# Kernel tuning notes

Hardware: AMD Instinct MI355X
Metric: run time of the kernel (lower is better)

The kernel has to match this reference:

```python
import jax, jax.numpy as jnp
import numpy as np

# dims (see shape_source)
N = 20000      # spots / graph nodes
G = 3000       # genes
NF = 256       # NFeature = CrossAttention dim
D_IN = 256     # dims_spot[0]
HID = 64       # dims_spot[1]
OUT = 16       # dims_spot[2]
H = 3          # GATv2 heads
E1 = 640000
E2 = 320000
SLOPE = 0.2    # leaky relu negative slope (GATv2 + CrossAttention alpha)


def _gat_params(key, din, hid, heads):
    k = jax.random.split(key, 3)
    s = 1.0 / np.sqrt(din)
    Wl = jax.random.normal(k[0], (din, heads * hid), jnp.float32) * s
    Wr = jax.random.normal(k[1], (din, heads * hid), jnp.float32) * s
    att = jax.random.normal(k[2], (heads, hid), jnp.float32) * s
    bl = jnp.zeros((heads * hid,), jnp.float32)
    br = jnp.zeros((heads * hid,), jnp.float32)
    b = jnp.zeros((hid,), jnp.float32)
    return Wl, bl, Wr, br, att, b


def setup_inputs() -> dict:
    key = jax.random.key(0)
    ks = jax.random.split(key, 16)
    inp = {
        "gene_freq_mtx": jax.random.normal(ks[0], (NF, G), jnp.float32),
        "gene_eigvecs_T": jax.random.normal(ks[1], (G, N), jnp.float32) / np.sqrt(G),
        "spot_freq_mtx": jax.random.normal(ks[2], (N, D_IN), jnp.float32),
        "spot_eigvecs_T": jax.random.normal(ks[3], (D_IN, NF), jnp.float32) / np.sqrt(D_IN),
        "spotnet": jax.random.randint(ks[4], (2, E1), 0, N, jnp.int32),
        "spotnet_cluster": jax.random.randint(ks[5], (2, E2), 0, N, jnp.int32),
    }
    for name, din, kk in [("c1", D_IN, ks[6]), ("c1p", D_IN, ks[7]), ("c3", OUT, ks[8]), ("c3p", OUT, ks[9])]:
        Wl, bl, Wr, br, att, b = _gat_params(kk, din, HID, H)
        inp[name + "_Wl"] = Wl; inp[name + "_bl"] = bl
        inp[name + "_Wr"] = Wr; inp[name + "_br"] = br
        inp[name + "_att"] = att; inp[name + "_b"] = b
    inp["W2"] = jax.random.normal(ks[10], (2 * HID, OUT), jnp.float32) / np.sqrt(2 * HID)
    inp["b2"] = jnp.zeros((OUT,), jnp.float32)
    inp["W4"] = jax.random.normal(ks[11], (2 * HID, D_IN), jnp.float32) / np.sqrt(2 * HID)
    inp["b4"] = jnp.zeros((D_IN,), jnp.float32)
    inp["a1"] = jax.random.normal(ks[12], (2 * NF, 1), jnp.float32) * 0.05
    inp["a2"] = jax.random.normal(ks[13], (2 * NF, 1), jnp.float32) * 0.05
    return inp


def gatv2(x, edge_index, Wl, bl, Wr, br, att, b, n):
    """PyG GATv2Conv, concat=False (head mean), add_self_loops=False, eval mode."""
    heads, c = att.shape
    src, dst = edge_index[0], edge_index[1]
    xl = (x @ Wl + bl).reshape(-1, heads, c)   # source transform [N,H,C]
    xr = (x @ Wr + br).reshape(-1, heads, c)   # target transform [N,H,C]
    m = jax.nn.leaky_relu(xl[src] + xr[dst], SLOPE)          # [E,H,C]
    e = jnp.einsum('ehc,hc->eh', m, att)                      # [E,H]
    emax = jax.ops.segment_max(e, dst, num_segments=n)        # [N,H]
    emax = jnp.where(jnp.isfinite(emax), emax, 0.0)           # empty segments
    p = jnp.exp(e - emax[dst])
    denom = jax.ops.segment_sum(p, dst, num_segments=n)       # [N,H]
    alpha = p / jnp.maximum(denom, 1e-16)[dst]                # segment softmax
    out = jax.ops.segment_sum(alpha[:, :, None] * xl[src], dst, num_segments=n)
    return out.mean(axis=1) + b                                # [N,C]


def reference(gene_freq_mtx, gene_eigvecs_T, spot_freq_mtx, spot_eigvecs_T,
              c1_Wl, c1_bl, c1_Wr, c1_br, c1_att, c1_b,
              c1p_Wl, c1p_bl, c1p_Wr, c1p_br, c1p_att, c1p_b,
              W2, b2,
              c3_Wl, c3_bl, c3_Wr, c3_br, c3_att, c3_b,
              c3p_Wl, c3p_bl, c3p_Wr, c3p_br, c3p_att, c3p_b,
              W4, b4, a1, a2, spotnet, spotnet_cluster):
    n = spot_freq_mtx.shape[0]
    # GAT (cluster=True)
    h1n = gatv2(spot_freq_mtx, spotnet, c1_Wl, c1_bl, c1_Wr, c1_br, c1_att, c1_b, n)
    h1p = gatv2(spot_freq_mtx, spotnet_cluster, c1p_Wl, c1p_bl, c1p_Wr, c1p_br, c1p_att, c1p_b, n)
    h1 = jax.nn.elu(jnp.concatenate([h1n, h1p], axis=1))
    h2 = h1 @ W2 + b2                                          # emb_spot [N,OUT]
    h3n = gatv2(h2, spotnet, c3_Wl, c3_bl, c3_Wr, c3_br, c3_att, c3_b, n)
    h3p = gatv2(h2, spotnet_cluster, c3p_Wl, c3p_bl, c3p_Wr, c3p_br, c3p_att, c3p_b, n)
    h3 = jax.nn.elu(jnp.concatenate([h3n, h3p], axis=1))
    h4 = h3 @ W4 + b4                                          # mtx_res_spot [N,D_IN]
    # iGFT + clip-at-zero (== relu)
    Xg = jax.nn.relu(gene_eigvecs_T.T @ gene_freq_mtx.T)       # [N,NF]
    Xs = jax.nn.relu(h4 @ spot_eigvecs_T)                      # [N,NF]
    # CrossAttention (dropout=0.0)
    cat = jnp.concatenate([Xg, Xs], axis=1)                    # [N,2NF]
    e = jax.nn.leaky_relu(jnp.concatenate([cat @ a1, cat @ a2], axis=1), SLOPE)
    lam = jax.nn.softmax(e, axis=1)                            # [N,2]
    res = lam[:, :1] * Xg + lam[:, 1:] * Xs
    return (res, lam, h2, h4)
```

## Files before the change

### kernel.cpp

```cpp
#include <hip/hip_runtime.h>

typedef unsigned short u16;
typedef __attribute__((ext_vector_type(8))) short bf16x8;
typedef __attribute__((ext_vector_type(4))) float floatx4;

#define NSPOT 20000
#define NGENE 3000
#define E1N   640000
#define E2N   320000

#define OFF_RES 0
#define OFF_LAM 5120000
#define OFF_H2  5160000
#define OFF_H4  5480000

__device__ __forceinline__ float b2f(u16 u){
  union { unsigned int i; float f; } v; v.i = ((unsigned int)u) << 16; return v.f;
}
__device__ __forceinline__ u16 f2b(float f){
  union { float f; unsigned int i; } v; v.f = f;
  unsigned int i = v.i;
  return (u16)((i + 0x7FFFu + ((i >> 16) & 1u)) >> 16);
}
__device__ __forceinline__ void stout(void* O, size_t i, float v, int isbf){
  if (isbf) ((u16*)O)[i] = f2b(v); else ((float*)O)[i] = v;
}
__device__ __forceinline__ u16 ldu(const void* p, size_t i, int isbf){
  return isbf ? ((const u16*)p)[i] : f2b(((const float*)p)[i]);
}

__global__ void sniff_kernel(const u16* __restrict__ x, int* __restrict__ flag){
  int lane = threadIdx.x;
  u16 u = x[lane * 2];
  int e = (u >> 7) & 0xFF;
  int sane = (u == 0) || (e >= 0x60 && e <= 0xA0);
  unsigned long long b = __ballot(sane);
  if (lane == 0) flag[0] = (__popcll(b) >= 48) ? 1 : 0;
}

struct ConvSeg { const void* src; u16* dst; int n; };
struct ConvBatch { ConvSeg s[14]; };
__global__ void convbatch_kernel(ConvBatch cb, const int* __restrict__ dflag){
  ConvSeg S = cb.s[blockIdx.y];
  int i = blockIdx.x * 256 + threadIdx.x;
  if (i < S.n) S.dst[i] = ldu(S.src, i, dflag[0]);
}

__global__ void conv3_kernel(const void* __restrict__ s0, u16* __restrict__ d0, int n0,
                             const void* __restrict__ s1, u16* __restrict__ d1, int n1,
                             const void* __restrict__ s2, u16* __restrict__ d2, int n2,
                             const int* __restrict__ dflag){
  int i = blockIdx.x * 256 + threadIdx.x;
  const void* src; u16* dst; int local;
  if (i < n0){ src = s0; dst = d0; local = i; }
  else if (i < n0 + n1){ src = s1; dst = d1; local = i - n0; }
  else if (i < n0 + n1 + n2){ src = s2; dst = d2; local = i - n0 - n1; }
  else return;
  size_t b = (size_t)local * 4;
  u16 o[4];
  if (dflag[0]){
    *(uint2*)o = *(const uint2*)((const u16*)src + b);
  } else {
    float4 f = *(const float4*)((const float*)src + b);
    o[0]=f2b(f.x); o[1]=f2b(f.y); o[2]=f2b(f.z); o[3]=f2b(f.w);
  }
  *(uint2*)(dst + b) = *(uint2*)o;
}

__global__ __launch_bounds__(256) void transpose_kernel(
    const void* __restrict__ GE, u16* __restrict__ AT,
    const int* __restrict__ dflag, int K, int M){
  __shared__ float tile[64 * 65];
  int isbf = dflag[0];
  int m0 = blockIdx.x * 64, k0 = blockIdx.y * 64;
#pragma unroll
  for (int i = 0; i < 4; i++){
    int idx = threadIdx.x + i * 256;
    int kr = idx >> 4, mc = (idx & 15) * 4;
    int gk = k0 + kr, gm = m0 + mc;
    if (gk < K){
      float v0 = 0.f, v1 = 0.f, v2 = 0.f, v3 = 0.f;
      if (gm + 4 <= M){
        if (isbf){
          const u16* pp = (const u16*)GE + (size_t)gk * M + gm;
          v0 = b2f(pp[0]); v1 = b2f(pp[1]); v2 = b2f(pp[2]); v3 = b2f(pp[3]);
        } else {
          float4 f = *(const float4*)((const float*)GE + (size_t)gk * M + gm);
          v0 = f.x; v1 = f.y; v2 = f.z; v3 = f.w;
        }
      } else {
        for (int e = 0; e < 4; e++){
          if (gm + e < M){
            float t = isbf ? b2f(((const u16*)GE)[(size_t)gk * M + gm + e])
                           : ((const float*)GE)[(size_t)gk * M + gm + e];
            if (e == 0) v0 = t; else if (e == 1) v1 = t; else if (e == 2) v2 = t; else v3 = t;
          }
        }
      }
      tile[(mc + 0) * 65 + kr] = v0;
      tile[(mc + 1) * 65 + kr] = v1;
      tile[(mc + 2) * 65 + kr] = v2;
      tile[(mc + 3) * 65 + kr] = v3;
    }
  }
  __syncthreads();
#pragma unroll
  for (int i = 0; i < 2; i++){
    int idx = threadIdx.x + i * 256;
    int mr = idx >> 3, kc = (idx & 7) * 8;
    int gm = m0 + mr, gk = k0 + kc;
    if (gm < M && gk < K){
      if (gk + 8 <= K){
        u16 o[8];
#pragma unroll
        for (int e = 0; e < 8; e++) o[e] = f2b(tile[mr * 65 + kc + e]);
        *(uint4*)&AT[(size_t)gm * K + gk] = *(uint4*)o;
      } else {
        for (int e = 0; e < 8 && gk + e < K; e++)
          AT[(size_t)gm * K + gk + e] = f2b(tile[mr * 65 + kc + e]);
      }
    }
  }
}

__global__ void hist2_kernel(const int* __restrict__ dst0, int E0, int* __restrict__ cnt0,
                             const int* __restrict__ dst1, int E1, int* __restrict__ cnt1){
  const int* dst = blockIdx.y ? dst1 : dst0;
  int* cnt = blockIdx.y ? cnt1 : cnt0;
  int E = blockIdx.y ? E1 : E0;
  int e = blockIdx.x * 256 + threadIdx.x;
  if (e < E){ int d = dst[e]; if ((unsigned)d < (unsigned)NSPOT) atomicAdd(&cnt[d], 1); }
}

__global__ void scan2_kernel(const int* __restrict__ c0, int* __restrict__ o0, int* __restrict__ u0,
                             const int* __restrict__ c1, int* __restrict__ o1, int* __restrict__ u1,
                             int n){
  const int* cnt = blockIdx.x ? c1 : c0;
  int* off = blockIdx.x ? o1 : o0;
  int* cur = blockIdx.x ? u1 : u0;
  __shared__ int part[256];
  int tid = threadIdx.x;
  int chunk = (n + 255) / 256;
  int lo = tid * chunk; if (lo > n) lo = n;
  int hi = lo + chunk; if (hi > n) hi = n;
  int s = 0;
  for (int i = lo; i < hi; i++) s += cnt[i];
  part[tid] = s;
  __syncthreads();
  if (tid == 0){
    int run = 0;
    for (int i = 0; i < 256; i++){ int t = part[i]; part[i] = run; run += t; }
  }
  __syncthreads();
  int run = part[tid];
  for (int i = lo; i < hi; i++){ off[i] = run; cur[i] = run; run += cnt[i]; }
  if (hi == n) off[n] = run;
}

__global__ void scatter2_kernel(const int* __restrict__ src0, const int* __restrict__ dst0,
                                int* __restrict__ cur0, int* __restrict__ out0, int E0,
                                const int* __restrict__ src1, const int* __restrict__ dst1,
                                int* __restrict__ cur1, int* __restrict__ out1, int E1){
  const int* src = blockIdx.y ? src1 : src0;
  const int* dst = blockIdx.y ? dst1 : dst0;
  int* cur = blockIdx.y ? cur1 : cur0;
  int* out = blockIdx.y ? out1 : out0;
  int E = blockIdx.y ? E1 : E0;
  int e = blockIdx.x * 256 + threadIdx.x;
  if (e < E){
    int d = dst[e];
    if ((unsigned)d < (unsigned)NSPOT){
      int p = atomicAdd(&cur[d], 1);
      if ((unsigned)p < (unsigned)E) out[p] = src[e];
    }
  }
}

struct AsmSet {
  const void *Wl, *bl, *Wr, *br, *Wlp, *blp, *Wrp, *brp;
  u16* Wcat; u16* bcat; int Kdim;
};
__global__ void assemble2_kernel(AsmSet s0, AsmSet s1, const int* __restrict__ dflag){
  AsmSet S = blockIdx.y ? s1 : s0;
  int isbf = dflag[0];
  int idx = blockIdx.x * 256 + threadIdx.x;
  int total = S.Kdim * 768;
  if (idx < total){
    int k = idx / 768, j = idx % 768;
    int seg = j / 192, jj = j % 192;
    const void* W = (seg == 0) ? S.Wl : (seg == 1) ? S.Wr : (seg == 2) ? S.Wlp : S.Wrp;
    S.Wcat[idx] = ldu(W, (size_t)k * 192 + jj, isbf);
  }
  if (idx < 768){
    int seg = idx / 192, jj = idx % 192;
    const void* b = (seg == 0) ? S.bl : (seg == 1) ? S.br : (seg == 2) ? S.blp : S.brp;
    S.bcat[idx] = ldu(b, jj, isbf);
  }
}

template<int BMI, bool A_KM, bool B_NK, bool A_EXT, bool B_EXT, bool RELU, bool HAS_BIAS, bool C_OUT, bool C2>
__global__ __launch_bounds__(256) void gemm_mfma(
    const void* __restrict__ A, const void* __restrict__ B,
    const u16* __restrict__ bias, void* __restrict__ Cp, u16* __restrict__ Cp2,
    const int* __restrict__ dflag, size_t aoff, size_t coff,
    int M, int N, int K, int lda, int ldb, int ldc, int ldc2)
{
  const int isbf = dflag[0];
  constexpr int BM = 64 * BMI, BK = 32, LDA = BK + 8, LDB = BK + 8;
  __shared__ __align__(16) u16 As[BM * LDA];
  __shared__ __align__(16) u16 Bs[64 * LDB];
  const u16*   A16 = (const u16*)A + aoff;
  const float* A32 = (const float*)A + aoff;
  const u16*   B16 = (const u16*)B;
  const float* B32 = (const float*)B;
  auto ldA = [&](size_t i) -> u16 { return (!A_EXT || isbf) ? A16[i] : f2b(A32[i]); };
  auto ldB = [&](size_t i) -> u16 { return (!B_EXT || isbf) ? B16[i] : f2b(B32[i]); };

  int tid = threadIdx.x;
  int lane = tid & 63, w = tid >> 6;
  int m0 = blockIdx.y * BM, n0 = blockIdx.x * 64;
  floatx4 acc[BMI][4] = {};
  int quad = lane >> 4;
  int nk = (K + BK - 1) / BK;
  for (int kt = 0; kt < nk; kt++){
    int k0 = kt * BK;
    if (!A_KM){
#pragma unroll
      for (int i = 0; i < BMI; i++){
        int id = tid + i * 256;
        int r = id >> 2, c = (id & 3) * 8;
        int gm = m0 + r, gk = k0 + c;
        if (gm < M && gk + 8 <= K){
          if (!A_EXT || isbf){
            *(uint4*)&As[r * LDA + c] = *(const uint4*)(A16 + (size_t)gm * lda + gk);
          } else {
            const float* p = A32 + (size_t)gm * lda + gk;
            float4 f0 = *(const float4*)p, f1 = *(const float4*)(p + 4);
            u16* d = &As[r * LDA + c];
            d[0]=f2b(f0.x); d[1]=f2b(f0.y); d[2]=f2b(f0.z); d[3]=f2b(f0.w);
            d[4]=f2b(f1.x); d[5]=f2b(f1.y); d[6]=f2b(f1.z); d[7]=f2b(f1.w);
          }
        } else {
          for (int e = 0; e < 8; e++)
            As[r * LDA + c + e] = (gm < M && gk + e < K) ? ldA((size_t)gm * lda + gk + e) : (u16)0;
        }
      }
    } else {
#pragma unroll
      for (int i = 0; i < BMI; i++){
        int id = tid + i * 256;
        int kk, rr;
        if (BMI == 2){ kk = id >> 4; rr = (id & 15) * 8; }
        else         { kk = id >> 3; rr = (id & 7) * 8; }
        int gk = k0 + kk, gm = m0 + rr;
        if (gk < K && gm + 8 <= M){
          if (!A_EXT || isbf){
            uint4 v = *(const uint4*)(A16 + (size_t)gk * lda + gm);
            const u16* pv = (const u16*)&v;
#pragma unroll
            for (int e = 0; e < 8; e++) As[(rr + e) * LDA + kk] = pv[e];
          } else {
            const float* p = A32 + (size_t)gk * lda + gm;
            float4 f0 = *(const float4*)p, f1 = *(const float4*)(p + 4);
            As[(rr+0)*LDA+kk]=f2b(f0.x); As[(rr+1)*LDA+kk]=f2b(f0.y);
            As[(rr+2)*LDA+kk]=f2b(f0.z); As[(rr+3)*LDA+kk]=f2b(f0.w);
            As[(rr+4)*LDA+kk]=f2b(f1.x); As[(rr+5)*LDA+kk]=f2b(f1.y);
            As[(rr+6)*LDA+kk]=f2b(f1.z); As[(rr+7)*LDA+kk]=f2b(f1.w);
          }
        } else {
          for (int e = 0; e < 8; e++)
            As[(rr + e) * LDA + kk] = (gk < K && gm + e < M) ? ldA((size_t)gk * lda + gm + e) : (u16)0;
        }
      }
    }
    if (B_NK){
      int r = tid >> 2, c = (tid & 3) * 8;
      int gn = n0 + r, gk = k0 + c;
      if (gn < N && gk + 8 <= K){
        if (!B_EXT || isbf){
          *(uint4*)&Bs[r * LDB + c] = *(const uint4*)(B16 + (size_t)gn * ldb + gk);
        } else {
          const float* p = B32 + (size_t)gn * ldb + gk;
          float4 f0 = *(const float4*)p, f1 = *(const float4*)(p + 4);
          u16* d = &Bs[r * LDB + c];
          d[0]=f2b(f0.x); d[1]=f2b(f0.y); d[2]=f2b(f0.z); d[3]=f2b(f0.w);
          d[4]=f2b(f1.x); d[5]=f2b(f1.y); d[6]=f2b(f1.z); d[7]=f2b(f1.w);
        }
      } else {
        for (int e = 0; e < 8; e++)
          Bs[r * LDB + c + e] = (gn < N && gk + e < K) ? ldB((size_t)gn * ldb + gk + e) : (u16)0;
      }
    } else {
      int kk = tid >> 3, nn = (tid & 7) * 8;
      int gk = k0 + kk, gn = n0 + nn;
      if (gk < K && gn + 8 <= N){
        if (!B_EXT || isbf){
          uint4 v = *(const uint4*)(B16 + (size_t)gk * ldb + gn);
          const u16* pv = (const u16*)&v;
#pragma unroll
          for (int e = 0; e < 8; e++) Bs[(nn + e) * LDB + kk] = pv[e];
        } else {
          const float* p = B32 + (size_t)gk * ldb + gn;
          float4 f0 = *(const float4*)p, f1 = *(const float4*)(p + 4);
          Bs[(nn+0)*LDB+kk]=f2b(f0.x); Bs[(nn+1)*LDB+kk]=f2b(f0.y);
          Bs[(nn+2)*LDB+kk]=f2b(f0.z); Bs[(nn+3)*LDB+kk]=f2b(f0.w);
          Bs[(nn+4)*LDB+kk]=f2b(f1.x); Bs[(nn+5)*LDB+kk]=f2b(f1.y);
          Bs[(nn+6)*LDB+kk]=f2b(f1.z); Bs[(nn+7)*LDB+kk]=f2b(f1.w);
        }
      } else {
        for (int e = 0; e < 8; e++)
          Bs[(nn + e) * LDB + kk] = (gk < K && gn + e < N) ? ldB((size_t)gk * ldb + gn + e) : (u16)0;
      }
    }
    __syncthreads();
    bf16x8 af[BMI];
#pragma unroll
    for (int mi = 0; mi < BMI; mi++)
      af[mi] = *(const bf16x8*)&As[(w * (16 * BMI) + mi * 16 + (lane & 15)) * LDA + quad * 8];
#pragma unroll
    for (int ni = 0; ni < 4; ni++){
      bf16x8 bfr = *(const bf16x8*)&Bs[(ni * 16 + (lane & 15)) * LDB + quad * 8];
#pragma unroll
      for (int mi = 0; mi < BMI; mi++)
        acc[mi][ni] = __builtin_amdgcn_mfma_f32_16x16x32_bf16(af[mi], bfr, acc[mi][ni], 0, 0, 0);
    }
    __syncthreads();
  }
#pragma unroll
  for (int mi = 0; mi < BMI; mi++)
#pragma unroll
    for (int ni = 0; ni < 4; ni++)
#pragma unroll
      for (int r = 0; r < 4; r++){
        int row = m0 + w * (16 * BMI) + mi * 16 + quad * 4 + r;
        int col = n0 + ni * 16 + (lane & 15);
        if (row < M && col < N){
          float v = acc[mi][ni][r];
          if (HAS_BIAS) v += b2f(bias[col]);
          if (RELU) v = fmaxf(v, 0.f);
          size_t ci = coff + (size_t)row * ldc + col;
          if (!C_OUT) ((u16*)Cp)[ci] = f2b(v);
          else stout(Cp, ci, v, isbf);
          if (C2) Cp2[(size_t)row * ldc2 + col] = f2b(v);
        }
      }
}

struct GatSet {
  const int* off; const int* srcs; const u16* att; const u16* bias;
  int xl_off, xr_off, out_off, E;
};
__global__ __launch_bounds__(256) void gat2_kernel(
    const u16* __restrict__ Y, GatSet SA, GatSet SB,
    u16* __restrict__ aggout, int n)
{
  int half = gridDim.x >> 1;
  int selB = (int)blockIdx.x >= half;
  GatSet S = selB ? SB : SA;
  int bx = blockIdx.x - (selB ? half : 0);
  int wid = (bx * 256 + threadIdx.x) >> 6;
  int lane = threadIdx.x & 63;
  if (wid >= n) return;
  int sub = lane >> 4;
  int cbase = (lane & 15) * 4;
  const int ldY = 768;
  size_t drow = (size_t)wid * ldY;

  float xr[3][4], at[3][4];
#pragma unroll
  for (int h = 0; h < 3; h++){
    uint2 vx = *(const uint2*)(Y + drow + S.xr_off + h * 64 + cbase);
    uint2 va = *(const uint2*)(S.att + h * 64 + cbase);
    const u16* px = (const u16*)&vx;
    const u16* pa = (const u16*)&va;
#pragma unroll
    for (int j = 0; j < 4; j++){ xr[h][j] = b2f(px[j]); at[h][j] = b2f(pa[j]); }
  }

  int beg = S.off[wid], end = S.off[wid + 1];
  beg = max(0, min(beg, S.E));
  end = max(beg, min(end, S.E));

  float mh[3] = {-INFINITY, -INFINITY, -INFINITY};
  float lh[3] = {0.f, 0.f, 0.f};
  float ac[3][4] = {};

  uint2 xa[3] = {};
  int s_b = 0;
  if (beg < end){
    int e0 = beg + sub;
    int s = (e0 < end) ? S.srcs[e0] : 0;
    if ((unsigned)s >= (unsigned)NSPOT) s = 0;
    const u16* p = Y + (size_t)s * ldY + S.xl_off + cbase;
#pragma unroll
    for (int h = 0; h < 3; h++) xa[h] = *(const uint2*)(p + h * 64);
    if (beg + 4 < end){
      int e1 = beg + 4 + sub;
      int s1 = (e1 < end) ? S.srcs[e1] : 0;
      if ((unsigned)s1 >= (unsigned)NSPOT) s1 = 0;
      s_b = s1;
    }
  }

  for (int b = beg; b < end; b += 4){
    uint2 xc[3];
#pragma unroll
    for (int h = 0; h < 3; h++) xc[h] = xa[h];
    bool act = (b + sub) < end;

    if (b + 4 < end){
      const u16* p = Y + (size_t)s_b * ldY + S.xl_off + cbase;
#pragma unroll
      for (int h = 0; h < 3; h++) xa[h] = *(const uint2*)(p + h * 64);
      if (b + 8 < end){
        int e2 = b + 8 + sub;
        int s2 = (e2 < end) ? S.srcs[e2] : 0;
        if ((unsigned)s2 >= (unsigned)NSPOT) s2 = 0;
        s_b = s2;
      }
    }

    float xl[3][4];
    float t0, t1, t2;
    {
      float a0 = 0.f, a1 = 0.f, a2 = 0.f;
      const u16* p0 = (const u16*)&xc[0];
      const u16* p1 = (const u16*)&xc[1];
      const u16* p2 = (const u16*)&xc[2];
#pragma unroll
      for (int j = 0; j < 4; j++){
        float x0 = b2f(p0[j]); xl[0][j] = x0;
        float u0 = x0 + xr[0][j]; u0 = fmaxf(u0, 0.2f * u0);
        a0 = __builtin_fmaf(at[0][j], u0, a0);
        float x1 = b2f(p1[j]); xl[1][j] = x1;
        float u1 = x1 + xr[1][j]; u1 = fmaxf(u1, 0.2f * u1);
        a1 = __builtin_fmaf(at[1][j], u1, a1);
        float x2 = b2f(p2[j]); xl[2][j] = x2;
        float u2 = x2 + xr[2][j]; u2 = fmaxf(u2, 0.2f * u2);
        a2 = __builtin_fmaf(at[2][j], u2, a2);
      }
      t0 = a0; t1 = a1; t2 = a2;
    }
#pragma unroll
    for (int d = 1; d < 16; d <<= 1){
      t0 += __shfl_xor(t0, d, 64);
      t1 += __shfl_xor(t1, d, 64);
      t2 += __shfl_xor(t2, d, 64);
    }
    if (act){
      float tt[3] = {t0, t1, t2};
#pragma unroll
      for (int h = 0; h < 3; h++){
        float nm = fmaxf(mh[h], tt[h]);
        if (nm > mh[h]){
          float sc = __expf(mh[h] - nm);
          lh[h] *= sc;
#pragma unroll
          for (int j = 0; j < 4; j++) ac[h][j] *= sc;
          mh[h] = nm;
        }
        float w = __expf(tt[h] - mh[h]);
        lh[h] += w;
#pragma unroll
        for (int j = 0; j < 4; j++) ac[h][j] = __builtin_fmaf(w, xl[h][j], ac[h][j]);
      }
    }
  }

  float o[4] = {0.f, 0.f, 0.f, 0.f};
#pragma unroll
  for (int h = 0; h < 3; h++){
    float gm = fmaxf(mh[h], __shfl_xor(mh[h], 16, 64));
    gm = fmaxf(gm, __shfl_xor(gm, 32, 64));
    float sc = (mh[h] == -INFINITY) ? 0.f : __expf(mh[h] - gm);
    float L = lh[h] * sc;
    L += __shfl_xor(L, 16, 64);
    L += __shfl_xor(L, 32, 64);
    float inv = 1.f / fmaxf(L, 1e-16f);
#pragma unroll
    for (int j = 0; j < 4; j++){
      float a = ac[h][j] * sc;
      a += __shfl_xor(a, 16, 64);
      a += __shfl_xor(a, 32, 64);
      o[j] += a * inv;
    }
  }
  if (sub == 0){
    u16 ov[4];
#pragma unroll
    for (int j = 0; j < 4; j++){
      float v = o[j] * (1.f / 3.f) + b2f(S.bias[cbase + j]);
      v = (v > 0.f) ? v : expm1f(v);
      if (!(fabsf(v) < 1e30f)) v = 0.f;
      ov[j] = f2b(v);
    }
    *(uint2*)&aggout[(size_t)wid * 128 + S.out_off + cbase] = *(uint2*)ov;
  }
}

__global__ __launch_bounds__(256) void h2y2_kernel(
    const u16* __restrict__ AGG, const u16* __restrict__ W2, const u16* __restrict__ b2,
    const u16* __restrict__ Wcat2, const u16* __restrict__ bcat2,
    void* __restrict__ OUT, u16* __restrict__ Y2,
    const int* __restrict__ dflag, int n){
  __shared__ float w2s[128 * 16];
  __shared__ float as_[16][128];
  __shared__ float h[16][16];
  __shared__ __align__(16) u16 ws_[16 * 768];
  int isbf = dflag[0];
  int tid = threadIdx.x;
  for (int i = tid; i < 128 * 16; i += 256) w2s[i] = b2f(W2[i]);
  for (int i = tid; i < 1536; i += 256) ((uint4*)ws_)[i] = ((const uint4*)Wcat2)[i];
  int m0 = blockIdx.x * 16;
  for (int i = tid; i < 16 * 128; i += 256){
    int r = i >> 7, c = i & 127; int m = m0 + r;
    as_[r][c] = (m < n) ? b2f(AGG[(size_t)m * 128 + c]) : 0.f;
  }
  __syncthreads();
  {
    int r = tid >> 4, j = tid & 15;
    int m = m0 + r;
    float acc = b2f(b2[j]);
    for (int k = 0; k < 128; k++) acc += as_[r][k] * w2s[k * 16 + j];
    h[r][j] = acc;
    if (m < n) stout(OUT, (size_t)OFF_H2 + (size_t)m * 16 + j, acc, isbf);
  }
  __syncthreads();
  int j = tid;
  float acc[16][3];
  float bj0 = b2f(bcat2[j]), bj1 = b2f(bcat2[j + 256]), bj2 = b2f(bcat2[j + 512]);
#pragma unroll
  for (int r = 0; r < 16; r++){ acc[r][0] = bj0; acc[r][1] = bj1; acc[r][2] = bj2; }
  for (int k = 0; k < 16; k++){
    float w0 = b2f(ws_[k * 768 + j]);
    float w1 = b2f(ws_[k * 768 + j + 256]);
    float w2 = b2f(ws_[k * 768 + j + 512]);
#pragma unroll
    for (int r = 0; r < 16; r++){
      float hv = h[r][k];
      acc[r][0] += hv * w0; acc[r][1] += hv * w1; acc[r][2] += hv * w2;
    }
  }
#pragma unroll
  for (int r = 0; r < 16; r++){
    int m = m0 + r;
    if (m < n){
      size_t base = (size_t)m * 768;
      Y2[base + j] = f2b(acc[r][0]);
      Y2[base + j + 256] = f2b(acc[r][1]);
      Y2[base + j + 512] = f2b(acc[r][2]);
    }
  }
}

__global__ __launch_bounds__(256) void cross_attn_kernel(
    const u16* __restrict__ XG, const u16* __restrict__ XS,
    const u16* __restrict__ a1, const u16* __restrict__ a2,
    void* __restrict__ OUT, const int* __restrict__ dflag, int n){
  int wid = (blockIdx.x * 256 + threadIdx.x) >> 6;
  int lane = threadIdx.x & 63;
  if (wid >= n) return;
  int isbf = dflag[0];
  int c0 = lane * 4;
  size_t base = (size_t)wid * 256 + c0;
  float g[4], s[4];
#pragma unroll
  for (int e = 0; e < 4; e++){ g[e] = b2f(XG[base + e]); s[e] = b2f(XS[base + e]); }
  float p1 = 0.f, p2 = 0.f;
#pragma unroll
  for (int e = 0; e < 4; e++){
    p1 += g[e] * b2f(a1[c0 + e]) + s[e] * b2f(a1[256 + c0 + e]);
    p2 += g[e] * b2f(a2[c0 + e]) + s[e] * b2f(a2[256 + c0 + e]);
  }
#pragma unroll
  for (int d = 32; d > 0; d >>= 1){
    p1 += __shfl_xor(p1, d, 64);
    p2 += __shfl_xor(p2, d, 64);
  }
  float e1 = (p1 > 0.f) ? p1 : 0.2f * p1;
  float e2 = (p2 > 0.f) ? p2 : 0.2f * p2;
  float mx = fmaxf(e1, e2);
  float w1 = __expf(e1 - mx), w2 = __expf(e2 - mx);
  float inv = 1.f / (w1 + w2);
  float l0 = w1 * inv, l1 = w2 * inv;
#pragma unroll
  for (int e = 0; e < 4; e++)
    stout(OUT, (size_t)OFF_RES + base + e, l0 * g[e] + l1 * s[e], isbf);
  if (lane == 0){
    stout(OUT, (size_t)OFF_LAM + (size_t)wid * 2,     l0, isbf);
    stout(OUT, (size_t)OFF_LAM + (size_t)wid * 2 + 1, l1, isbf);
  }
}

extern "C" void kernel_launch(void* const* d_in, const int* in_sizes, int n_in,
                              void* d_out, int out_size, void* d_ws, size_t ws_size,
                              hipStream_t stream) {
  const void* gene_freq = d_in[0];
  const void* gene_eig  = d_in[1];
  const void* spot_freq = d_in[2];
  const void* spot_eig  = d_in[3];
  const int* net1 = (const int*)d_in[4];
  const int* net2 = (const int*)d_in[5];
  const void *c1_Wl=d_in[6],  *c1_bl=d_in[7],  *c1_Wr=d_in[8],  *c1_br=d_in[9],  *c1_att=d_in[10], *c1_b=d_in[11];
  const void *c1p_Wl=d_in[12],*c1p_bl=d_in[13],*c1p_Wr=d_in[14],*c1p_br=d_in[15],*c1p_att=d_in[16],*c1p_b=d_in[17];
  const void *c3_Wl=d_in[18], *c3_bl=d_in[19], *c3_Wr=d_in[20], *c3_br=d_in[21], *c3_att=d_in[22], *c3_b=d_in[23];
  const void *c3p_Wl=d_in[24],*c3p_bl=d_in[25],*c3p_Wr=d_in[26],*c3p_br=d_in[27],*c3p_att=d_in[28],*c3p_b=d_in[29];
  const void *W2=d_in[30], *b2=d_in[31], *W4=d_in[32], *b4=d_in[33], *a1=d_in[34], *a2=d_in[35];

  char* p0 = (char*)d_ws;
  char* p = p0;
  auto carve = [&](size_t bytes) -> char* {
    char* r = p; p += (bytes + 255) & ~(size_t)255; return r;
  };
  int*   flag  = (int*) carve(256);
  int*   cnt1  = (int*) carve((NSPOT + 2) * 4);
  int*   off1  = (int*) carve((NSPOT + 2) * 4);
  int*   cur1  = (int*) carve((NSPOT + 2) * 4);
  int*   srcs1 = (int*) carve((size_t)E1N * 4);
  int*   cnt2  = (int*) carve((NSPOT + 2) * 4);
  int*   off2  = (int*) carve((NSPOT + 2) * 4);
  int*   cur2  = (int*) carve((NSPOT + 2) * 4);
  int*   srcs2 = (int*) carve((size_t)E2N * 4);
  u16*   Wcat1 = (u16*) carve(256 * 768 * 2);
  u16*   bcat1 = (u16*) carve(2048);
  u16*   Wcat2 = (u16*) carve(16 * 768 * 2);
  u16*   bcat2 = (u16*) carve(2048);
  u16*   attc1  = (u16*)carve(192 * 2);
  u16*   attc1p = (u16*)carve(192 * 2);
  u16*   attc3  = (u16*)carve(192 * 2);
  u16*   attc3p = (u16*)carve(192 * 2);
  u16*   bc1  = (u16*)carve(64 * 2);
  u16*   bc1p = (u16*)carve(64 * 2);
  u16*   bc3  = (u16*)carve(64 * 2);
  u16*   bc3p = (u16*)carve(64 * 2);
  u16*   W2c  = (u16*)carve(2048 * 2);
  u16*   b2c  = (u16*)carve(16 * 2);
  u16*   W4c  = (u16*)carve(32768 * 2);
  u16*   b4c  = (u16*)carve(256 * 2);
  u16*   a1c  = (u16*)carve(512 * 2);
  u16*   a2c  = (u16*)carve(512 * 2);
  u16*   GF16 = (u16*) carve((size_t)256 * 3000 * 2);
  u16*   SE16 = (u16*) carve((size_t)256 * 256 * 2);
  u16*   SF16 = (u16*) carve((size_t)NSPOT * 256 * 2);
  u16*   H4B  = (u16*) carve((size_t)NSPOT * 256 * 2);
  u16*   AGG  = (u16*) carve((size_t)NSPOT * 128 * 2);
  u16*   XGp  = (u16*) carve((size_t)NSPOT * 256 * 2);
  char*  R    = carve(0);
  size_t used_common = (size_t)(R - p0);
  size_t needA = used_common + (size_t)NSPOT * NGENE * 2
               + (size_t)NSPOT * 768 * 2
               + (size_t)NSPOT * 256 * 2
               + 4096;
  bool planA = (ws_size >= needA);

  sniff_kernel<<<1, 64, 0, stream>>>((const u16*)spot_freq, flag);
  hipMemsetAsync(cnt1, 0, NSPOT * 4, stream);
  hipMemsetAsync(cnt2, 0, NSPOT * 4, stream);
  hist2_kernel<<<dim3((E1N + 255) / 256, 2), 256, 0, stream>>>(
      net1 + E1N, E1N, cnt1, net2 + E2N, E2N, cnt2);
  scan2_kernel<<<2, 256, 0, stream>>>(cnt1, off1, cur1, cnt2, off2, cur2, NSPOT);
  scatter2_kernel<<<dim3((E1N + 255) / 256, 2), 256, 0, stream>>>(
      net1, net1 + E1N, cur1, srcs1, E1N, net2, net2 + E2N, cur2, srcs2, E2N);

  ConvBatch cb;
  cb.s[0]  = {c1_att,  attc1,  192}; cb.s[1]  = {c1p_att, attc1p, 192};
  cb.s[2]  = {c3_att,  attc3,  192}; cb.s[3]  = {c3p_att, attc3p, 192};
  cb.s[4]  = {c1_b, bc1, 64}; cb.s[5]  = {c1p_b, bc1p, 64};
  cb.s[6]  = {c3_b, bc3, 64}; cb.s[7]  = {c3p_b, bc3p, 64};
  cb.s[8]  = {W2, W2c, 2048}; cb.s[9]  = {b2, b2c, 16};
  cb.s[10] = {W4, W4c, 32768}; cb.s[11] = {b4, b4c, 256};
  cb.s[12] = {a1, a1c, 512}; cb.s[13] = {a2, a2c, 512};
  convbatch_kernel<<<dim3(128, 14), 256, 0, stream>>>(cb, flag);

  {
    int n0 = 256 * 3000 / 4, n1 = 256 * 256 / 4, n2 = NSPOT * 256 / 4;
    int tot = n0 + n1 + n2;
    conv3_kernel<<<(tot + 255) / 256, 256, 0, stream>>>(
        gene_freq, GF16, n0, spot_eig, SE16, n1, spot_freq, SF16, n2, flag);
  }

  AsmSet as0 = {c1_Wl, c1_bl, c1_Wr, c1_br, c1p_Wl, c1p_bl, c1p_Wr, c1p_br, Wcat1, bcat1, 256};
  AsmSet as1 = {c3_Wl, c3_bl, c3_Wr, c3_br, c3p_Wl, c3p_bl, c3p_Wr, c3p_br, Wcat2, bcat2, 16};
  assemble2_kernel<<<dim3((256 * 768 + 255) / 256, 2), 256, 0, stream>>>(as0, as1, flag);

  GatSet g1a = {off1, srcs1, attc1,  bc1,  0,   192, 0,  E1N};
  GatSet g1b = {off2, srcs2, attc1p, bc1p, 384, 576, 64, E2N};
  GatSet g3a = {off1, srcs1, attc3,  bc3,  0,   192, 0,  E1N};
  GatSet g3b = {off2, srcs2, attc3p, bc3p, 384, 576, 64, E2N};

  u16* Y;
  u16* XS;
  u16* XG = XGp;
  if (planA){
    u16* AT = (u16*)R;
    Y  = (u16*)(R + (size_t)NSPOT * NGENE * 2);
    XS = Y + (size_t)NSPOT * 768;

    transpose_kernel<<<dim3(313, 47), 256, 0, stream>>>(gene_eig, AT, flag, NGENE, NSPOT);
    gemm_mfma<2, false, true, false, false, true, false, false, false><<<dim3(4, 157), 256, 0, stream>>>(
        AT, GF16, nullptr, XG, nullptr, flag, 0, 0, NSPOT, 256, NGENE, NGENE, NGENE, 256, 0);
  } else {
    Y  = (u16*)R;
    XS = Y + (size_t)NSPOT * 768;
    gemm_mfma<2, true, true, true, true, true, false, false, false><<<dim3(4, 157), 256, 0, stream>>>(
        gene_eig, gene_freq, nullptr, XG, nullptr, flag, 0, 0, NSPOT, 256, NGENE, NSPOT, NGENE, 256, 0);
  }

  gemm_mfma<2, false, false, false, false, false, true, false, false><<<dim3(12, 157), 256, 0, stream>>>(
      SF16, Wcat1, bcat1, Y, nullptr, flag, 0, 0, NSPOT, 768, 256, 256, 768, 768, 0);
  gat2_kernel<<<10000, 256, 0, stream>>>(Y, g1a, g1b, AGG, NSPOT);
  h2y2_kernel<<<1250, 256, 0, stream>>>(AGG, W2c, b2c, Wcat2, bcat2, d_out, Y, flag, NSPOT);
  gat2_kernel<<<10000, 256, 0, stream>>>(Y, g3a, g3b, AGG, NSPOT);
  gemm_mfma<2, false, false, false, false, false, true, true, true><<<dim3(4, 157), 256, 0, stream>>>(
      AGG, W4c, b4c, d_out, H4B, flag, 0, OFF_H4, NSPOT, 256, 128, 128, 256, 256, 256);
  gemm_mfma<2, false, false, false, false, true, false, false, false><<<dim3(4, 157), 256, 0, stream>>>(
      H4B, SE16, nullptr, XS, nullptr, flag, 0, 0, NSPOT, 256, 256, 256, 256, 256, 0);
  cross_attn_kernel<<<5000, 256, 0, stream>>>(XG, XS, a1c, a2c, d_out, flag, NSPOT);

  (void)in_sizes; (void)n_in; (void)out_size; (void)ws_size;
}
```

Before: 1.091 ms.

## Compute gene iGFT transposed with split-K, drop explicit transpose, widen GAT lanes

```diff
diff --git a/kernel.cpp b/kernel.cpp
--- a/kernel.cpp
+++ b/kernel.cpp
@@ -65,62 +65,6 @@
     o[0]=f2b(f.x); o[1]=f2b(f.y); o[2]=f2b(f.z); o[3]=f2b(f.w);
   }
   *(uint2*)(dst + b) = *(uint2*)o;
-}
-
-__global__ __launch_bounds__(256) void transpose_kernel(
-    const void* __restrict__ GE, u16* __restrict__ AT,
-    const int* __restrict__ dflag, int K, int M){
-  __shared__ float tile[64 * 65];
-  int isbf = dflag[0];
-  int m0 = blockIdx.x * 64, k0 = blockIdx.y * 64;
-#pragma unroll
-  for (int i = 0; i < 4; i++){
-    int idx = threadIdx.x + i * 256;
-    int kr = idx >> 4, mc = (idx & 15) * 4;
-    int gk = k0 + kr, gm = m0 + mc;
-    if (gk < K){
-      float v0 = 0.f, v1 = 0.f, v2 = 0.f, v3 = 0.f;
-      if (gm + 4 <= M){
-        if (isbf){
-          const u16* pp = (const u16*)GE + (size_t)gk * M + gm;
-          v0 = b2f(pp[0]); v1 = b2f(pp[1]); v2 = b2f(pp[2]); v3 = b2f(pp[3]);
-        } else {
-          float4 f = *(const float4*)((const float*)GE + (size_t)gk * M + gm);
-          v0 = f.x; v1 = f.y; v2 = f.z; v3 = f.w;
-        }
-      } else {
-        for (int e = 0; e < 4; e++){
-          if (gm + e < M){
-            float t = isbf ? b2f(((const u16*)GE)[(size_t)gk * M + gm + e])
-                           : ((const float*)GE)[(size_t)gk * M + gm + e];
-            if (e == 0) v0 = t; else if (e == 1) v1 = t; else if (e == 2) v2 = t; else v3 = t;
-          }
-        }
-      }
-      tile[(mc + 0) * 65 + kr] = v0;
-      tile[(mc + 1) * 65 + kr] = v1;
-      tile[(mc + 2) * 65 + kr] = v2;
-      tile[(mc + 3) * 65 + kr] = v3;
-    }
-  }
-  __syncthreads();
-#pragma unroll
-  for (int i = 0; i < 2; i++){
-    int idx = threadIdx.x + i * 256;
-    int mr = idx >> 3, kc = (idx & 7) * 8;
-    int gm = m0 + mr, gk = k0 + kc;
-    if (gm < M && gk < K){
-      if (gk + 8 <= K){
-        u16 o[8];
-#pragma unroll
-        for (int e = 0; e < 8; e++) o[e] = f2b(tile[mr * 65 + kc + e]);
-        *(uint4*)&AT[(size_t)gm * K + gk] = *(uint4*)o;
-      } else {
-        for (int e = 0; e < 8 && gk + e < K; e++)
-          AT[(size_t)gm * K + gk + e] = f2b(tile[mr * 65 + kc + e]);
-      }
-    }
-  }
 }
 
 __global__ void hist2_kernel(const int* __restrict__ dst0, int E0, int* __restrict__ cnt0,
@@ -198,12 +142,13 @@
   }
 }
 
-template<int BMI, bool A_KM, bool B_NK, bool A_EXT, bool B_EXT, bool RELU, bool HAS_BIAS, bool C_OUT, bool C2>
+template<int BMI, bool A_KM, bool B_NK, bool A_EXT, bool B_EXT, bool RELU, bool HAS_BIAS, bool C_OUT, bool C2, bool C_F32>
 __global__ __launch_bounds__(256) void gemm_mfma(
     const void* __restrict__ A, const void* __restrict__ B,
     const u16* __restrict__ bias, void* __restrict__ Cp, u16* __restrict__ Cp2,
     const int* __restrict__ dflag, size_t aoff, size_t coff,
-    int M, int N, int K, int lda, int ldb, int ldc, int ldc2)
+    int M, int N, int K, int kchunk, size_t cstride,
+    int lda, int ldb, int ldc, int ldc2)
 {
   const int isbf = dflag[0];
   constexpr int BM = 64 * BMI, BK = 32, LDA = BK + 8, LDB = BK + 8;
@@ -219,11 +164,13 @@
   int tid = threadIdx.x;
   int lane = tid & 63, w = tid >> 6;
   int m0 = blockIdx.y * BM, n0 = blockIdx.x * 64;
+  int kbeg = (int)blockIdx.z * kchunk;
+  int kend = (K < kbeg + kchunk) ? K : (kbeg + kchunk);
   floatx4 acc[BMI][4] = {};
   int quad = lane >> 4;
-  int nk = (K + BK - 1) / BK;
+  int nk = (kend - kbeg + BK - 1) / BK;
   for (int kt = 0; kt < nk; kt++){
-    int k0 = kt * BK;
+    int k0 = kbeg + kt * BK;
     if (!A_KM){
 #pragma unroll
       for (int i = 0; i < BMI; i++){
@@ -338,12 +285,58 @@
           float v = acc[mi][ni][r];
           if (HAS_BIAS) v += b2f(bias[col]);
           if (RELU) v = fmaxf(v, 0.f);
-          size_t ci = coff + (size_t)row * ldc + col;
-          if (!C_OUT) ((u16*)Cp)[ci] = f2b(v);
+          size_t ci = coff + (size_t)blockIdx.z * cstride + (size_t)row * ldc + col;
+          if (C_F32) ((float*)Cp)[ci] = v;
+          else if (!C_OUT) ((u16*)Cp)[ci] = f2b(v);
           else stout(Cp, ci, v, isbf);
           if (C2) Cp2[(size_t)row * ldc2 + col] = f2b(v);
         }
       }
+}
+
+__global__ __launch_bounds__(256) void redtr_kernel(const float* __restrict__ P,
+                                                    u16* __restrict__ XG){
+  __shared__ float tile[64 * 65];
+  int s0 = blockIdx.x * 64;
+  int c0 = blockIdx.y * 64;
+  int t = threadIdx.x;
+#pragma unroll
+  for (int i = 0; i < 4; i++){
+    int c = i * 16 + (t >> 4);
+    int sp = (t & 15) * 4;
+    int gs = s0 + sp;
+    size_t base = (size_t)(c0 + c) * NSPOT + gs;
+    float v0 = 0.f, v1 = 0.f, v2 = 0.f, v3 = 0.f;
+    if (gs + 4 <= NSPOT){
+      float4 a = *(const float4*)(P + base);
+      float4 b = *(const float4*)(P + (size_t)256 * NSPOT + base);
+      v0 = a.x + b.x; v1 = a.y + b.y; v2 = a.z + b.z; v3 = a.w + b.w;
+    } else {
+      for (int e = 0; e < 4; e++){
+        if (gs + e < NSPOT){
+          float x = P[base + e] + P[(size_t)256 * NSPOT + base + e];
+          if (e == 0) v0 = x; else if (e == 1) v1 = x; else if (e == 2) v2 = x; else v3 = x;
+        }
+      }
+    }
+    tile[c * 65 + sp + 0] = fmaxf(v0, 0.f);
+    tile[c * 65 + sp + 1] = fmaxf(v1, 0.f);
+    tile[c * 65 + sp + 2] = fmaxf(v2, 0.f);
+    tile[c * 65 + sp + 3] = fmaxf(v3, 0.f);
+  }
+  __syncthreads();
+#pragma unroll
+  for (int i = 0; i < 2; i++){
+    int sp = i * 32 + (t >> 3);
+    int cc = (t & 7) * 8;
+    int gs = s0 + sp;
+    if (gs < NSPOT){
+      u16 o[8];
+#pragma unroll
+      for (int e = 0; e < 8; e++) o[e] = f2b(tile[(cc + e) * 65 + sp]);
+      *(uint4*)&XG[(size_t)gs * 256 + c0 + cc] = *(uint4*)o;
+    }
+  }
 }
 
 struct GatSet {
@@ -361,20 +354,20 @@
   int wid = (bx * 256 + threadIdx.x) >> 6;
   int lane = threadIdx.x & 63;
   if (wid >= n) return;
-  int sub = lane >> 4;
-  int cbase = (lane & 15) * 4;
+  int sub = lane >> 3;
+  int cbase = (lane & 7) * 8;
   const int ldY = 768;
   size_t drow = (size_t)wid * ldY;
 
-  float xr[3][4], at[3][4];
+  float xr[3][8], at[3][8];
 #pragma unroll
   for (int h = 0; h < 3; h++){
-    uint2 vx = *(const uint2*)(Y + drow + S.xr_off + h * 64 + cbase);
-    uint2 va = *(const uint2*)(S.att + h * 64 + cbase);
+    uint4 vx = *(const uint4*)(Y + drow + S.xr_off + h * 64 + cbase);
+    uint4 va = *(const uint4*)(S.att + h * 64 + cbase);
     const u16* px = (const u16*)&vx;
     const u16* pa = (const u16*)&va;
 #pragma unroll
-    for (int j = 0; j < 4; j++){ xr[h][j] = b2f(px[j]); at[h][j] = b2f(pa[j]); }
+    for (int j = 0; j < 8; j++){ xr[h][j] = b2f(px[j]); at[h][j] = b2f(pa[j]); }
   }
 
   int beg = S.off[wid], end = S.off[wid + 1];
@@ -383,9 +376,9 @@
 
   float mh[3] = {-INFINITY, -INFINITY, -INFINITY};
   float lh[3] = {0.f, 0.f, 0.f};
-  float ac[3][4] = {};
-
-  uint2 xa[3] = {};
+  float ac[3][8] = {};
+
+  uint4 xa[3] = {};
   int s_b = 0;
   if (beg < end){
     int e0 = beg + sub;
@@ -393,56 +386,54 @@
     if ((unsigned)s >= (unsigned)NSPOT) s = 0;
     const u16* p = Y + (size_t)s * ldY + S.xl_off + cbase;
 #pragma unroll
-    for (int h = 0; h < 3; h++) xa[h] = *(const uint2*)(p + h * 64);
-    if (beg + 4 < end){
-      int e1 = beg + 4 + sub;
+    for (int h = 0; h < 3; h++) xa[h] = *(const uint4*)(p + h * 64);
+    if (beg + 8 < end){
+      int e1 = beg + 8 + sub;
       int s1 = (e1 < end) ? S.srcs[e1] : 0;
       if ((unsigned)s1 >= (unsigned)NSPOT) s1 = 0;
       s_b = s1;
     }
   }
 
-  for (int b = beg; b < end; b += 4){
-    uint2 xc[3];
+  for (int b = beg; b < end; b += 8){
+    uint4 xc[3];
 #pragma unroll
     for (int h = 0; h < 3; h++) xc[h] = xa[h];
     bool act = (b + sub) < end;
 
-    if (b + 4 < end){
+    if (b + 8 < end){
       const u16* p = Y + (size_t)s_b * ldY + S.xl_off + cbase;
 #pragma unroll
-      for (int h = 0; h < 3; h++) xa[h] = *(const uint2*)(p + h * 64);
-      if (b + 8 < end){
-        int e2 = b + 8 + sub;
+      for (int h = 0; h < 3; h++) xa[h] = *(const uint4*)(p + h * 64);
+      if (b + 16 < end){
+        int e2 = b + 16 + sub;
         int s2 = (e2 < end) ? S.srcs[e2] : 0;
         if ((unsigned)s2 >= (unsigned)NSPOT) s2 = 0;
         s_b = s2;
       }
     }
 
-    float xl[3][4];
-    float t0, t1, t2;
+    float xl[3][8];
+    float t0 = 0.f, t1 = 0.f, t2 = 0.f;
     {
-      float a0 = 0.f, a1 = 0.f, a2 = 0.f;
       const u16* p0 = (const u16*)&xc[0];
       const u16* p1 = (const u16*)&xc[1];
       const u16* p2 = (const u16*)&xc[2];
 #pragma unroll
-      for (int j = 0; j < 4; j++){
+      for (int j = 0; j < 8; j++){
         float x0 = b2f(p0[j]); xl[0][j] = x0;
         float u0 = x0 + xr[0][j]; u0 = fmaxf(u0, 0.2f * u0);
-        a0 = __builtin_fmaf(at[0][j], u0, a0);
+        t0 = __builtin_fmaf(at[0][j], u0, t0);
         float x1 = b2f(p1[j]); xl[1][j] = x1;
         float u1 = x1 + xr[1][j]; u1 = fmaxf(u1, 0.2f * u1);
-        a1 = __builtin_fmaf(at[1][j], u1, a1);
+        t1 = __builtin_fmaf(at[1][j], u1, t1);
         float x2 = b2f(p2[j]); xl[2][j] = x2;
         float u2 = x2 + xr[2][j]; u2 = fmaxf(u2, 0.2f * u2);
-        a2 = __builtin_fmaf(at[2][j], u2, a2);
-      }
-      t0 = a0; t1 = a1; t2 = a2;
-    }
-#pragma unroll
-    for (int d = 1; d < 16; d <<= 1){
+        t2 = __builtin_fmaf(at[2][j], u2, t2);
+      }
+    }
+#pragma unroll
+    for (int d = 1; d < 8; d <<= 1){
       t0 += __shfl_xor(t0, d, 64);
       t1 += __shfl_xor(t1, d, 64);
       t2 += __shfl_xor(t2, d, 64);
@@ -456,45 +447,48 @@
           float sc = __expf(mh[h] - nm);
           lh[h] *= sc;
 #pragma unroll
-          for (int j = 0; j < 4; j++) ac[h][j] *= sc;
+          for (int j = 0; j < 8; j++) ac[h][j] *= sc;
           mh[h] = nm;
         }
         float w = __expf(tt[h] - mh[h]);
         lh[h] += w;
 #pragma unroll
-        for (int j = 0; j < 4; j++) ac[h][j] = __builtin_fmaf(w, xl[h][j], ac[h][j]);
-      }
-    }
-  }
-
-  float o[4] = {0.f, 0.f, 0.f, 0.f};
+        for (int j = 0; j < 8; j++) ac[h][j] = __builtin_fmaf(w, xl[h][j], ac[h][j]);
+      }
+    }
+  }
+
+  float o[8] = {};
 #pragma unroll
   for (int h = 0; h < 3; h++){
-    float gm = fmaxf(mh[h], __shfl_xor(mh[h], 16, 64));
+    float gm = fmaxf(mh[h], __shfl_xor(mh[h], 8, 64));
+    gm = fmaxf(gm, __shfl_xor(gm, 16, 64));
     gm = fmaxf(gm, __shfl_xor(gm, 32, 64));
     float sc = (mh[h] == -INFINITY) ? 0.f : __expf(mh[h] - gm);
     float L = lh[h] * sc;
+    L += __shfl_xor(L, 8, 64);
     L += __shfl_xor(L, 16, 64);
     L += __shfl_xor(L, 32, 64);
     float inv = 1.f / fmaxf(L, 1e-16f);
 #pragma unroll
-    for (int j = 0; j < 4; j++){
+    for (int j = 0; j < 8; j++){
       float a = ac[h][j] * sc;
+      a += __shfl_xor(a, 8, 64);
       a += __shfl_xor(a, 16, 64);
       a += __shfl_xor(a, 32, 64);
       o[j] += a * inv;
     }
   }
   if (sub == 0){
-    u16 ov[4];
-#pragma unroll
-    for (int j = 0; j < 4; j++){
+    u16 ov[8];
+#pragma unroll
+    for (int j = 0; j < 8; j++){
       float v = o[j] * (1.f / 3.f) + b2f(S.bias[cbase + j]);
       v = (v > 0.f) ? v : expm1f(v);
       if (!(fabsf(v) < 1e30f)) v = 0.f;
       ov[j] = f2b(v);
     }
-    *(uint2*)&aggout[(size_t)wid * 128 + S.out_off + cbase] = *(uint2*)ov;
+    *(uint4*)&aggout[(size_t)wid * 128 + S.out_off + cbase] = *(uint4*)ov;
   }
 }
 
@@ -644,14 +638,11 @@
   u16*   SF16 = (u16*) carve((size_t)NSPOT * 256 * 2);
   u16*   H4B  = (u16*) carve((size_t)NSPOT * 256 * 2);
   u16*   AGG  = (u16*) carve((size_t)NSPOT * 128 * 2);
-  u16*   XGp  = (u16*) carve((size_t)NSPOT * 256 * 2);
-  char*  R    = carve(0);
-  size_t used_common = (size_t)(R - p0);
-  size_t needA = used_common + (size_t)NSPOT * NGENE * 2
-               + (size_t)NSPOT * 768 * 2
-               + (size_t)NSPOT * 256 * 2
-               + 4096;
-  bool planA = (ws_size >= needA);
+  u16*   XG   = (u16*) carve((size_t)NSPOT * 256 * 2);
+  char*  R    = carve((size_t)2 * 256 * NSPOT * 4);
+  float* Pbuf = (float*)R;
+  u16*   Y    = (u16*)R;
+  u16*   XS   = (u16*)(R + (size_t)NSPOT * 768 * 2);
 
   sniff_kernel<<<1, 64, 0, stream>>>((const u16*)spot_freq, flag);
   hipMemsetAsync(cnt1, 0, NSPOT * 4, stream);
@@ -688,33 +679,27 @@
   GatSet g3a = {off1, srcs1, attc3,  bc3,  0,   192, 0,  E1N};
   GatSet g3b = {off2, srcs2, attc3p, bc3p, 384, 576, 64, E2N};
 
-  u16* Y;
-  u16* XS;
-  u16* XG = XGp;
-  if (planA){
-    u16* AT = (u16*)R;
-    Y  = (u16*)(R + (size_t)NSPOT * NGENE * 2);
-    XS = Y + (size_t)NSPOT * 768;
-
-    transpose_kernel<<<dim3(313, 47), 256, 0, stream>>>(gene_eig, AT, flag, NGENE, NSPOT);
-    gemm_mfma<2, false, true, false, false, true, false, false, false><<<dim3(4, 157), 256, 0, stream>>>(
-        AT, GF16, nullptr, XG, nullptr, flag, 0, 0, NSPOT, 256, NGENE, NGENE, NGENE, 256, 0);
-  } else {
-    Y  = (u16*)R;
-    XS = Y + (size_t)NSPOT * 768;
-    gemm_mfma<2, true, true, true, true, true, false, false, false><<<dim3(4, 157), 256, 0, stream>>>(
-        gene_eig, gene_freq, nullptr, XG, nullptr, flag, 0, 0, NSPOT, 256, NGENE, NSPOT, NGENE, 256, 0);
-  }
-
-  gemm_mfma<2, false, false, false, false, false, true, false, false><<<dim3(12, 157), 256, 0, stream>>>(
-      SF16, Wcat1, bcat1, Y, nullptr, flag, 0, 0, NSPOT, 768, 256, 256, 768, 768, 0);
+  gemm_mfma<2, false, false, false, true, false, false, false, false, true>
+      <<<dim3(313, 2, 2), 256, 0, stream>>>(
+      GF16, gene_eig, nullptr, Pbuf, nullptr, flag, 0, 0,
+      256, NSPOT, NGENE, 1504, (size_t)256 * NSPOT, NGENE, NSPOT, NSPOT, 0);
+  redtr_kernel<<<dim3(313, 4), 256, 0, stream>>>(Pbuf, XG);
+
+  gemm_mfma<2, false, false, false, false, false, true, false, false, false>
+      <<<dim3(12, 157), 256, 0, stream>>>(
+      SF16, Wcat1, bcat1, Y, nullptr, flag, 0, 0,
+      NSPOT, 768, 256, 256, 0, 256, 768, 768, 0);
   gat2_kernel<<<10000, 256, 0, stream>>>(Y, g1a, g1b, AGG, NSPOT);
   h2y2_kernel<<<1250, 256, 0, stream>>>(AGG, W2c, b2c, Wcat2, bcat2, d_out, Y, flag, NSPOT);
   gat2_kernel<<<10000, 256, 0, stream>>>(Y, g3a, g3b, AGG, NSPOT);
-  gemm_mfma<2, false, false, false, false, false, true, true, true><<<dim3(4, 157), 256, 0, stream>>>(
-      AGG, W4c, b4c, d_out, H4B, flag, 0, OFF_H4, NSPOT, 256, 128, 128, 256, 256, 256);
-  gemm_mfma<2, false, false, false, false, true, false, false, false><<<dim3(4, 157), 256, 0, stream>>>(
-      H4B, SE16, nullptr, XS, nullptr, flag, 0, 0, NSPOT, 256, 256, 256, 256, 256, 0);
+  gemm_mfma<1, false, false, false, false, false, true, true, true, false>
+      <<<dim3(4, 313), 256, 0, stream>>>(
+      AGG, W4c, b4c, d_out, H4B, flag, 0, OFF_H4,
+      NSPOT, 256, 128, 128, 0, 128, 256, 256, 256);
+  gemm_mfma<1, false, false, false, false, true, false, false, false, false>
+      <<<dim3(4, 313), 256, 0, stream>>>(
+      H4B, SE16, nullptr, XS, nullptr, flag, 0, 0,
+      NSPOT, 256, 256, 256, 0, 256, 256, 256, 0);
   cross_attn_kernel<<<5000, 256, 0, stream>>>(XG, XS, a1c, a2c, d_out, flag, NSPOT);
 
   (void)in_sizes; (void)n_in; (void)out_size; (void)ws_size;
```

Result: faster. 1.024 ms (-6.1%).
